# Performance work log

Hardware: AMD Instinct MI355X
Metric: run time of the kernel (lower is better)

## Reference

```python
import jax, jax.numpy as jnp
import numpy as np

N = 512  # DFT size, fixed by the module


def _dft_weights():
    # W[h, j] = exp(-2i*pi*j*h/N), same as the torch init loop
    h = np.arange(N).reshape(N, 1).astype(np.float64)
    j = np.arange(N).reshape(1, N).astype(np.float64)
    ang = -2.0 * np.pi * (h * j) / N
    return np.cos(ang).astype(np.float32), np.sin(ang).astype(np.float32)


def setup_inputs() -> dict:
    key = jax.random.key(0)
    k1, k2 = jax.random.split(key)
    shape = (8, 16, 256, N)  # (batch, channels, doppler, range_samples)
    x_re = jax.random.normal(k1, shape, dtype=jnp.float32)
    x_im = jax.random.normal(k2, shape, dtype=jnp.float32)
    w_re, w_im = _dft_weights()
    return {
        "x_re": x_re,
        "x_im": x_im,
        "w_re": jnp.asarray(w_re),
        "w_im": jnp.asarray(w_im),
    }


def reference(x_re, x_im, w_re, w_im):
    # CplxLinear without bias: y = x @ W^T, complex.
    # y_re = x_re @ Wr^T - x_im @ Wi^T ; y_im = x_re @ Wi^T + x_im @ Wr^T
    y_re = jnp.einsum('bcdj,hj->bcdh', x_re, w_re) - jnp.einsum('bcdj,hj->bcdh', x_im, w_im)
    y_im = jnp.einsum('bcdj,hj->bcdh', x_re, w_im) + jnp.einsum('bcdj,hj->bcdh', x_im, w_re)
    # stack real/imag on trailing axis (equivalent to torch.view_as_real layout)
    return jnp.stack([y_re, y_im], axis=-1)
```

## Files before the change

kernel.cpp:

```cpp
#include <hip/hip_runtime.h>

typedef __bf16 bf16_t;
typedef __bf16 bf16x8 __attribute__((ext_vector_type(8)));
typedef float f32x4 __attribute__((ext_vector_type(4)));
typedef unsigned int u32x4 __attribute__((ext_vector_type(4)));

#define KDIM 512
#define NDIM 512
#define BM 128
#define BN 128
#define BK 32

__device__ __forceinline__ void gld_lds16(const float* g, float* lds_uniform) {
  __builtin_amdgcn_global_load_lds(
      (const __attribute__((address_space(1))) void*)g,
      (__attribute__((address_space(3))) void*)lds_uniform, 16, 0, 0);
}

__device__ __forceinline__ bf16x8 neg8(bf16x8 v) {
  union { bf16x8 b; u32x4 u; } x;
  x.b = v;
  x.u = x.u ^ 0x80008000u;
  return x.b;
}

__device__ __forceinline__ bf16x8 afrag(const float* ldsx, int r, int h4) {
  const int base = r * 8;
  const int sw = r & 7;
  const float4 a = *(const float4*)(ldsx + 4 * (base + ((2 * h4) ^ sw)));
  const float4 b = *(const float4*)(ldsx + 4 * (base + ((2 * h4 + 1) ^ sw)));
  bf16x8 f;
  f[0] = (__bf16)a.x; f[1] = (__bf16)a.y; f[2] = (__bf16)a.z; f[3] = (__bf16)a.w;
  f[4] = (__bf16)b.x; f[5] = (__bf16)b.y; f[6] = (__bf16)b.z; f[7] = (__bf16)b.w;
  return f;
}

__device__ __forceinline__ bf16x8 pack8(float4 a, float4 b) {
  bf16x8 f;
  f[0] = (__bf16)a.x; f[1] = (__bf16)a.y; f[2] = (__bf16)a.z; f[3] = (__bf16)a.w;
  f[4] = (__bf16)b.x; f[5] = (__bf16)b.y; f[6] = (__bf16)b.z; f[7] = (__bf16)b.w;
  return f;
}

__global__ __launch_bounds__(256, 2) void dft_cgemm_kernel(
    const float* __restrict__ xr, const float* __restrict__ xi,
    const float* __restrict__ wre, const float* __restrict__ wim,
    float* __restrict__ out) {
  __shared__ __align__(16) float lds_xr[BM * BK];
  __shared__ __align__(16) float lds_xi[BM * BK];
  __shared__ __align__(16) bf16_t lds_wr[BN * BK];
  __shared__ __align__(16) bf16_t lds_wi[BN * BK];

  const int t = threadIdx.x;
  const int lane = t & 63;
  const int wv = t >> 6;

  const int b = blockIdx.x;
  const int xcd = b & 7;
  const int sidx = b >> 3;
  const int m0 = (xcd * 32 + (sidx >> 2)) * BM;
  const int n0 = (sidx & 3) * BN;

  const int wm = (wv >> 1) * 64;
  const int wn = (wv & 1) * 64;
  const int l16 = lane & 15;
  const int h4 = lane >> 4;

  const int wt15 = t & 15;
  const int wg = (t >> 4) & 3;

  f32x4 acc_re[4][4], acc_im[4][4];
#pragma unroll
  for (int i = 0; i < 4; ++i)
#pragma unroll
    for (int j = 0; j < 4; ++j) {
      acc_re[i][j] = (f32x4){0.f, 0.f, 0.f, 0.f};
      acc_im[i][j] = (f32x4){0.f, 0.f, 0.f, 0.f};
    }

  for (int k0 = 0; k0 < KDIM; k0 += BK) {
#pragma unroll
    for (int it = 0; it < 4; ++it) {
      const int S = it * 256 + t;
      const int row = S >> 3;
      const int g = (S & 7) ^ (row & 7);
      const size_t goff = (size_t)(m0 + row) * KDIM + k0 + g * 4;
      float* dst_r = lds_xr + 4 * (it * 256 + wv * 64);
      float* dst_i = lds_xi + 4 * (it * 256 + wv * 64);
      gld_lds16(xr + goff, dst_r);
      gld_lds16(xi + goff, dst_i);
    }
#pragma unroll
    for (int c = 0; c < 2; ++c) {
      const int row = (c * 4 + wv) * 16 + wt15;
      const float* gr = wre + (size_t)(n0 + row) * KDIM + k0 + wg * 8;
      const float* gi = wim + (size_t)(n0 + row) * KDIM + k0 + wg * 8;
      const float4 r0 = ((const float4*)gr)[0];
      const float4 r1 = ((const float4*)gr)[1];
      const float4 i0 = ((const float4*)gi)[0];
      const float4 i1 = ((const float4*)gi)[1];
      const int slot = c * 256 + t;
      *(bf16x8*)(lds_wr + slot * 8) = pack8(r0, r1);
      *(bf16x8*)(lds_wi + slot * 8) = pack8(i0, i1);
    }
    __syncthreads();

    bf16x8 ar[4], ai[4], br[4], bi[4], nbi[4];
#pragma unroll
    for (int mi = 0; mi < 4; ++mi) {
      const int r = wm + mi * 16 + l16;
      ar[mi] = afrag(lds_xr, r, h4);
      ai[mi] = afrag(lds_xi, r, h4);
    }
#pragma unroll
    for (int ni = 0; ni < 4; ++ni) {
      const int slot = ((wn >> 4) + ni) * 64 + h4 * 16 + l16;
      br[ni] = *(const bf16x8*)(lds_wr + slot * 8);
      bi[ni] = *(const bf16x8*)(lds_wi + slot * 8);
      nbi[ni] = neg8(bi[ni]);
    }
#pragma unroll
    for (int mi = 0; mi < 4; ++mi) {
#pragma unroll
      for (int ni = 0; ni < 4; ++ni) {
        acc_re[mi][ni] = __builtin_amdgcn_mfma_f32_16x16x32_bf16(ar[mi], br[ni], acc_re[mi][ni], 0, 0, 0);
        acc_im[mi][ni] = __builtin_amdgcn_mfma_f32_16x16x32_bf16(ar[mi], bi[ni], acc_im[mi][ni], 0, 0, 0);
        acc_re[mi][ni] = __builtin_amdgcn_mfma_f32_16x16x32_bf16(ai[mi], nbi[ni], acc_re[mi][ni], 0, 0, 0);
        acc_im[mi][ni] = __builtin_amdgcn_mfma_f32_16x16x32_bf16(ai[mi], br[ni], acc_im[mi][ni], 0, 0, 0);
      }
    }
    __syncthreads();
  }

#pragma unroll
  for (int mi = 0; mi < 4; ++mi) {
#pragma unroll
    for (int r = 0; r < 4; ++r) {
      const int m = m0 + wm + mi * 16 + h4 * 4 + r;
#pragma unroll
      for (int ni = 0; ni < 4; ++ni) {
        const int h = n0 + wn + ni * 16 + l16;
        float2 v;
        v.x = acc_re[mi][ni][r];
        v.y = acc_im[mi][ni][r];
        *(float2*)(out + ((size_t)m * NDIM + h) * 2) = v;
      }
    }
  }
}

extern "C" void kernel_launch(void* const* d_in, const int* in_sizes, int n_in,
                              void* d_out, int out_size, void* d_ws, size_t ws_size,
                              hipStream_t stream) {
  const float* xr  = (const float*)d_in[0];
  const float* xi  = (const float*)d_in[1];
  const float* wre = (const float*)d_in[2];
  const float* wim = (const float*)d_in[3];
  float* out = (float*)d_out;

  dim3 grid(1024);
  dim3 block(256);
  dft_cgemm_kernel<<<grid, block, 0, stream>>>(xr, xi, wre, wim, out);
}
```

Measured before the change: 293.8 us.

## Double-buffer X tiles in LDS and prefetch W into registers a step ahead

New measurement: 454.5 us. +54.7%, slower.

```diff
diff --git a/kernel.cpp b/kernel.cpp
--- a/kernel.cpp
+++ b/kernel.cpp
@@ -10,6 +10,7 @@
 #define BM 128
 #define BN 128
 #define BK 32
+#define NSTEP (KDIM / BK)
 
 __device__ __forceinline__ void gld_lds16(const float* g, float* lds_uniform) {
   __builtin_amdgcn_global_load_lds(
@@ -42,14 +43,14 @@
   return f;
 }
 
+struct Wregs { float4 r0, r1, i0, i1, r2, r3, i2, i3; };
+
 __global__ __launch_bounds__(256, 2) void dft_cgemm_kernel(
     const float* __restrict__ xr, const float* __restrict__ xi,
     const float* __restrict__ wre, const float* __restrict__ wim,
     float* __restrict__ out) {
-  __shared__ __align__(16) float lds_xr[BM * BK];
-  __shared__ __align__(16) float lds_xi[BM * BK];
-  __shared__ __align__(16) bf16_t lds_wr[BN * BK];
-  __shared__ __align__(16) bf16_t lds_wi[BN * BK];
+  __shared__ __align__(16) float  lds_x[2][2][BM * BK];
+  __shared__ __align__(16) bf16_t lds_w[2][BN * BK];
 
   const int t = threadIdx.x;
   const int lane = t & 63;
@@ -65,7 +66,6 @@
   const int wn = (wv & 1) * 64;
   const int l16 = lane & 15;
   const int h4 = lane >> 4;
-
   const int wt15 = t & 15;
   const int wg = (t >> 4) & 3;
 
@@ -78,45 +78,59 @@
       acc_im[i][j] = (f32x4){0.f, 0.f, 0.f, 0.f};
     }
 
-  for (int k0 = 0; k0 < KDIM; k0 += BK) {
+  auto stage_x = [&](int buf, int step) {
+    const int k0 = step * BK;
 #pragma unroll
     for (int it = 0; it < 4; ++it) {
       const int S = it * 256 + t;
       const int row = S >> 3;
       const int g = (S & 7) ^ (row & 7);
       const size_t goff = (size_t)(m0 + row) * KDIM + k0 + g * 4;
-      float* dst_r = lds_xr + 4 * (it * 256 + wv * 64);
-      float* dst_i = lds_xi + 4 * (it * 256 + wv * 64);
-      gld_lds16(xr + goff, dst_r);
-      gld_lds16(xi + goff, dst_i);
-    }
-#pragma unroll
-    for (int c = 0; c < 2; ++c) {
-      const int row = (c * 4 + wv) * 16 + wt15;
-      const float* gr = wre + (size_t)(n0 + row) * KDIM + k0 + wg * 8;
-      const float* gi = wim + (size_t)(n0 + row) * KDIM + k0 + wg * 8;
-      const float4 r0 = ((const float4*)gr)[0];
-      const float4 r1 = ((const float4*)gr)[1];
-      const float4 i0 = ((const float4*)gi)[0];
-      const float4 i1 = ((const float4*)gi)[1];
-      const int slot = c * 256 + t;
-      *(bf16x8*)(lds_wr + slot * 8) = pack8(r0, r1);
-      *(bf16x8*)(lds_wi + slot * 8) = pack8(i0, i1);
-    }
-    __syncthreads();
-
+      float* dr = &lds_x[buf][0][0] + 4 * (it * 256 + wv * 64);
+      float* di = &lds_x[buf][1][0] + 4 * (it * 256 + wv * 64);
+      gld_lds16(xr + goff, dr);
+      gld_lds16(xi + goff, di);
+    }
+  };
+
+  auto load_w = [&](int step) {
+    Wregs W;
+    const int k0 = step * BK;
+    const int row0 = wv * 16 + wt15;
+    const float* gr0 = wre + (size_t)(n0 + row0) * KDIM + k0 + wg * 8;
+    const float* gi0 = wim + (size_t)(n0 + row0) * KDIM + k0 + wg * 8;
+    W.r0 = ((const float4*)gr0)[0]; W.r1 = ((const float4*)gr0)[1];
+    W.i0 = ((const float4*)gi0)[0]; W.i1 = ((const float4*)gi0)[1];
+    const int row1 = 64 + wv * 16 + wt15;
+    const float* gr1 = wre + (size_t)(n0 + row1) * KDIM + k0 + wg * 8;
+    const float* gi1 = wim + (size_t)(n0 + row1) * KDIM + k0 + wg * 8;
+    W.r2 = ((const float4*)gr1)[0]; W.r3 = ((const float4*)gr1)[1];
+    W.i2 = ((const float4*)gi1)[0]; W.i3 = ((const float4*)gi1)[1];
+    return W;
+  };
+
+  auto write_w = [&](const Wregs& W) {
+    *(bf16x8*)(&lds_w[0][0] + (size_t)t * 8)         = pack8(W.r0, W.r1);
+    *(bf16x8*)(&lds_w[1][0] + (size_t)t * 8)         = pack8(W.i0, W.i1);
+    *(bf16x8*)(&lds_w[0][0] + (size_t)(256 + t) * 8) = pack8(W.r2, W.r3);
+    *(bf16x8*)(&lds_w[1][0] + (size_t)(256 + t) * 8) = pack8(W.i2, W.i3);
+  };
+
+  auto compute = [&](int buf) {
+    const float* ldsxr = &lds_x[buf][0][0];
+    const float* ldsxi = &lds_x[buf][1][0];
     bf16x8 ar[4], ai[4], br[4], bi[4], nbi[4];
 #pragma unroll
     for (int mi = 0; mi < 4; ++mi) {
       const int r = wm + mi * 16 + l16;
-      ar[mi] = afrag(lds_xr, r, h4);
-      ai[mi] = afrag(lds_xi, r, h4);
+      ar[mi] = afrag(ldsxr, r, h4);
+      ai[mi] = afrag(ldsxi, r, h4);
     }
 #pragma unroll
     for (int ni = 0; ni < 4; ++ni) {
       const int slot = ((wn >> 4) + ni) * 64 + h4 * 16 + l16;
-      br[ni] = *(const bf16x8*)(lds_wr + slot * 8);
-      bi[ni] = *(const bf16x8*)(lds_wi + slot * 8);
+      br[ni] = *(const bf16x8*)(&lds_w[0][0] + slot * 8);
+      bi[ni] = *(const bf16x8*)(&lds_w[1][0] + slot * 8);
       nbi[ni] = neg8(bi[ni]);
     }
 #pragma unroll
@@ -129,8 +143,52 @@
         acc_im[mi][ni] = __builtin_amdgcn_mfma_f32_16x16x32_bf16(ai[mi], br[ni], acc_im[mi][ni], 0, 0, 0);
       }
     }
-    __syncthreads();
+  };
+
+  Wregs Wp = load_w(0);
+  stage_x(0, 0);
+  write_w(Wp);
+  Wp = load_w(1);
+  stage_x(1, 1);
+  asm volatile("s_waitcnt vmcnt(16)" ::: "memory");
+  asm volatile("s_waitcnt lgkmcnt(0)" ::: "memory");
+  __builtin_amdgcn_s_barrier();
+  __builtin_amdgcn_sched_barrier(0);
+
+#pragma unroll 1
+  for (int tt = 0; tt < NSTEP - 2; tt += 2) {
+    compute(0);
+    __builtin_amdgcn_s_barrier();
+    __builtin_amdgcn_sched_barrier(0);
+    write_w(Wp);
+    Wp = load_w(tt + 2);
+    stage_x(0, tt + 2);
+    asm volatile("s_waitcnt vmcnt(16)" ::: "memory");
+    asm volatile("s_waitcnt lgkmcnt(0)" ::: "memory");
+    __builtin_amdgcn_s_barrier();
+    __builtin_amdgcn_sched_barrier(0);
+
+    compute(1);
+    __builtin_amdgcn_s_barrier();
+    __builtin_amdgcn_sched_barrier(0);
+    write_w(Wp);
+    Wp = load_w(tt + 3);
+    stage_x(1, tt + 3);
+    asm volatile("s_waitcnt vmcnt(16)" ::: "memory");
+    asm volatile("s_waitcnt lgkmcnt(0)" ::: "memory");
+    __builtin_amdgcn_s_barrier();
+    __builtin_amdgcn_sched_barrier(0);
   }
+
+  compute(0);
+  __builtin_amdgcn_s_barrier();
+  __builtin_amdgcn_sched_barrier(0);
+  write_w(Wp);
+  asm volatile("s_waitcnt vmcnt(0)" ::: "memory");
+  asm volatile("s_waitcnt lgkmcnt(0)" ::: "memory");
+  __builtin_amdgcn_s_barrier();
+  __builtin_amdgcn_sched_barrier(0);
+  compute(1);
 
 #pragma unroll
   for (int mi = 0; mi < 4; ++mi) {
```

## Load X fragments directly from global and stage W in larger K chunks

Applied to the files above, without the earlier changes.

After: 432.0 us. 47.1% more time.

```diff
diff --git a/kernel.cpp b/kernel.cpp
--- a/kernel.cpp
+++ b/kernel.cpp
@@ -10,29 +10,14 @@
 #define BM 128
 #define BN 128
 #define BK 32
-
-__device__ __forceinline__ void gld_lds16(const float* g, float* lds_uniform) {
-  __builtin_amdgcn_global_load_lds(
-      (const __attribute__((address_space(1))) void*)g,
-      (__attribute__((address_space(3))) void*)lds_uniform, 16, 0, 0);
-}
+#define KQ 128
+#define NQUART (KDIM / KQ)
 
 __device__ __forceinline__ bf16x8 neg8(bf16x8 v) {
   union { bf16x8 b; u32x4 u; } x;
   x.b = v;
   x.u = x.u ^ 0x80008000u;
   return x.b;
-}
-
-__device__ __forceinline__ bf16x8 afrag(const float* ldsx, int r, int h4) {
-  const int base = r * 8;
-  const int sw = r & 7;
-  const float4 a = *(const float4*)(ldsx + 4 * (base + ((2 * h4) ^ sw)));
-  const float4 b = *(const float4*)(ldsx + 4 * (base + ((2 * h4 + 1) ^ sw)));
-  bf16x8 f;
-  f[0] = (__bf16)a.x; f[1] = (__bf16)a.y; f[2] = (__bf16)a.z; f[3] = (__bf16)a.w;
-  f[4] = (__bf16)b.x; f[5] = (__bf16)b.y; f[6] = (__bf16)b.z; f[7] = (__bf16)b.w;
-  return f;
 }
 
 __device__ __forceinline__ bf16x8 pack8(float4 a, float4 b) {
@@ -46,10 +31,7 @@
     const float* __restrict__ xr, const float* __restrict__ xi,
     const float* __restrict__ wre, const float* __restrict__ wim,
     float* __restrict__ out) {
-  __shared__ __align__(16) float lds_xr[BM * BK];
-  __shared__ __align__(16) float lds_xi[BM * BK];
-  __shared__ __align__(16) bf16_t lds_wr[BN * BK];
-  __shared__ __align__(16) bf16_t lds_wi[BN * BK];
+  __shared__ __align__(16) bf16_t lds_w[2][BN * KQ];
 
   const int t = threadIdx.x;
   const int lane = t & 63;
@@ -65,9 +47,8 @@
   const int wn = (wv & 1) * 64;
   const int l16 = lane & 15;
   const int h4 = lane >> 4;
-
   const int wt15 = t & 15;
-  const int wg = (t >> 4) & 3;
+  const int wg16 = t >> 4;
 
   f32x4 acc_re[4][4], acc_im[4][4];
 #pragma unroll
@@ -78,58 +59,71 @@
       acc_im[i][j] = (f32x4){0.f, 0.f, 0.f, 0.f};
     }
 
-  for (int k0 = 0; k0 < KDIM; k0 += BK) {
+  auto stage_w = [&](int q) {
+    const int kq0 = q * KQ;
 #pragma unroll
-    for (int it = 0; it < 4; ++it) {
-      const int S = it * 256 + t;
-      const int row = S >> 3;
-      const int g = (S & 7) ^ (row & 7);
-      const size_t goff = (size_t)(m0 + row) * KDIM + k0 + g * 4;
-      float* dst_r = lds_xr + 4 * (it * 256 + wv * 64);
-      float* dst_i = lds_xi + 4 * (it * 256 + wv * 64);
-      gld_lds16(xr + goff, dst_r);
-      gld_lds16(xi + goff, dst_i);
-    }
-#pragma unroll
-    for (int c = 0; c < 2; ++c) {
-      const int row = (c * 4 + wv) * 16 + wt15;
-      const float* gr = wre + (size_t)(n0 + row) * KDIM + k0 + wg * 8;
-      const float* gi = wim + (size_t)(n0 + row) * KDIM + k0 + wg * 8;
+    for (int c = 0; c < 8; ++c) {
+      const int row = c * 16 + wt15;
+      const float* gr = wre + (size_t)(n0 + row) * KDIM + kq0 + wg16 * 8;
+      const float* gi = wim + (size_t)(n0 + row) * KDIM + kq0 + wg16 * 8;
       const float4 r0 = ((const float4*)gr)[0];
       const float4 r1 = ((const float4*)gr)[1];
       const float4 i0 = ((const float4*)gi)[0];
       const float4 i1 = ((const float4*)gi)[1];
       const int slot = c * 256 + t;
-      *(bf16x8*)(lds_wr + slot * 8) = pack8(r0, r1);
-      *(bf16x8*)(lds_wi + slot * 8) = pack8(i0, i1);
+      *(bf16x8*)(&lds_w[0][0] + (size_t)slot * 8) = pack8(r0, r1);
+      *(bf16x8*)(&lds_w[1][0] + (size_t)slot * 8) = pack8(i0, i1);
     }
-    __syncthreads();
+  };
 
-    bf16x8 ar[4], ai[4], br[4], bi[4], nbi[4];
+  stage_w(0);
+  __syncthreads();
+
+#pragma unroll 1
+  for (int q = 0; q < NQUART; ++q) {
 #pragma unroll
-    for (int mi = 0; mi < 4; ++mi) {
-      const int r = wm + mi * 16 + l16;
-      ar[mi] = afrag(lds_xr, r, h4);
-      ai[mi] = afrag(lds_xi, r, h4);
-    }
+    for (int ks = 0; ks < KQ / BK; ++ks) {
+      const int k0 = q * KQ + ks * BK;
+
+      bf16x8 ar[4], ai[4];
 #pragma unroll
-    for (int ni = 0; ni < 4; ++ni) {
-      const int slot = ((wn >> 4) + ni) * 64 + h4 * 16 + l16;
-      br[ni] = *(const bf16x8*)(lds_wr + slot * 8);
-      bi[ni] = *(const bf16x8*)(lds_wi + slot * 8);
-      nbi[ni] = neg8(bi[ni]);
-    }
-#pragma unroll
-    for (int mi = 0; mi < 4; ++mi) {
+      for (int mi = 0; mi < 4; ++mi) {
+        const size_t rbase =
+            (size_t)(m0 + wm + mi * 16 + l16) * KDIM + k0 + h4 * 8;
+        const float4 a0 = ((const float4*)(xr + rbase))[0];
+        const float4 a1 = ((const float4*)(xr + rbase))[1];
+        const float4 b0 = ((const float4*)(xi + rbase))[0];
+        const float4 b1 = ((const float4*)(xi + rbase))[1];
+        ar[mi] = pack8(a0, a1);
+        ai[mi] = pack8(b0, b1);
+      }
+
+      bf16x8 br[4], bi[4], nbi[4];
 #pragma unroll
       for (int ni = 0; ni < 4; ++ni) {
-        acc_re[mi][ni] = __builtin_amdgcn_mfma_f32_16x16x32_bf16(ar[mi], br[ni], acc_re[mi][ni], 0, 0, 0);
-        acc_im[mi][ni] = __builtin_amdgcn_mfma_f32_16x16x32_bf16(ar[mi], bi[ni], acc_im[mi][ni], 0, 0, 0);
-        acc_re[mi][ni] = __builtin_amdgcn_mfma_f32_16x16x32_bf16(ai[mi], nbi[ni], acc_re[mi][ni], 0, 0, 0);
-        acc_im[mi][ni] = __builtin_amdgcn_mfma_f32_16x16x32_bf16(ai[mi], br[ni], acc_im[mi][ni], 0, 0, 0);
+        const int slot = ((wn >> 4) + ni) * 256 + (ks * 4 + h4) * 16 + l16;
+        br[ni] = *(const bf16x8*)(&lds_w[0][0] + (size_t)slot * 8);
+        bi[ni] = *(const bf16x8*)(&lds_w[1][0] + (size_t)slot * 8);
+        nbi[ni] = neg8(bi[ni]);
+      }
+
+#pragma unroll
+      for (int mi = 0; mi < 4; ++mi) {
+#pragma unroll
+        for (int ni = 0; ni < 4; ++ni) {
+          acc_re[mi][ni] = __builtin_amdgcn_mfma_f32_16x16x32_bf16(ar[mi], br[ni], acc_re[mi][ni], 0, 0, 0);
+          acc_im[mi][ni] = __builtin_amdgcn_mfma_f32_16x16x32_bf16(ar[mi], bi[ni], acc_im[mi][ni], 0, 0, 0);
+          acc_re[mi][ni] = __builtin_amdgcn_mfma_f32_16x16x32_bf16(ai[mi], nbi[ni], acc_re[mi][ni], 0, 0, 0);
+          acc_im[mi][ni] = __builtin_amdgcn_mfma_f32_16x16x32_bf16(ai[mi], br[ni], acc_im[mi][ni], 0, 0, 0);
+        }
       }
     }
-    __syncthreads();
+
+    if (q + 1 < NQUART) {
+      __syncthreads();
+      stage_w(q + 1);
+      __syncthreads();
+    }
   }
 
 #pragma unroll
```

## Pre-pack DFT weights to bf16 and double-buffer LDS with async loads

Applied to the files above, without the earlier changes.

After: 317.8 us. +8.2%, slower.

```diff
diff --git a/kernel.cpp b/kernel.cpp
--- a/kernel.cpp
+++ b/kernel.cpp
@@ -10,6 +10,7 @@
 #define BM 128
 #define BN 128
 #define BK 32
+#define NSTEP (KDIM / BK)
 
 __device__ __forceinline__ void gld_lds16(const float* g, float* lds_uniform) {
   __builtin_amdgcn_global_load_lds(
@@ -24,25 +25,161 @@
   return x.b;
 }
 
+__device__ __forceinline__ bf16x8 pack8(float4 a, float4 b) {
+  bf16x8 f;
+  f[0] = (__bf16)a.x; f[1] = (__bf16)a.y; f[2] = (__bf16)a.z; f[3] = (__bf16)a.w;
+  f[4] = (__bf16)b.x; f[5] = (__bf16)b.y; f[6] = (__bf16)b.z; f[7] = (__bf16)b.w;
+  return f;
+}
+
 __device__ __forceinline__ bf16x8 afrag(const float* ldsx, int r, int h4) {
   const int base = r * 8;
   const int sw = r & 7;
   const float4 a = *(const float4*)(ldsx + 4 * (base + ((2 * h4) ^ sw)));
   const float4 b = *(const float4*)(ldsx + 4 * (base + ((2 * h4 + 1) ^ sw)));
-  bf16x8 f;
-  f[0] = (__bf16)a.x; f[1] = (__bf16)a.y; f[2] = (__bf16)a.z; f[3] = (__bf16)a.w;
-  f[4] = (__bf16)b.x; f[5] = (__bf16)b.y; f[6] = (__bf16)b.z; f[7] = (__bf16)b.w;
-  return f;
-}
-
-__device__ __forceinline__ bf16x8 pack8(float4 a, float4 b) {
-  bf16x8 f;
-  f[0] = (__bf16)a.x; f[1] = (__bf16)a.y; f[2] = (__bf16)a.z; f[3] = (__bf16)a.w;
-  f[4] = (__bf16)b.x; f[5] = (__bf16)b.y; f[6] = (__bf16)b.z; f[7] = (__bf16)b.w;
-  return f;
-}
-
-__global__ __launch_bounds__(256, 2) void dft_cgemm_kernel(
+  return pack8(a, b);
+}
+
+__global__ void dft_prep_w(const float* __restrict__ wre,
+                           const float* __restrict__ wim,
+                           bf16_t* __restrict__ wsw) {
+  const int gid = blockIdx.x * 256 + threadIdx.x;
+  const int comp = gid >> 15;
+  const int r15 = gid & 32767;
+  const int ntile = r15 >> 13;
+  const int r13 = r15 & 8191;
+  const int row = r13 >> 6;
+  const int sg = r13 & 63;
+  const int step = sg >> 2;
+  const int g = sg & 3;
+  const float* w = comp ? wim : wre;
+  const float* src = w + (size_t)(ntile * 128 + row) * KDIM + step * 32 + g * 8;
+  const float4 a = ((const float4*)src)[0];
+  const float4 b = ((const float4*)src)[1];
+  const int slot = (row >> 4) * 64 + g * 16 + (row & 15);
+  bf16_t* dst = wsw + ((((size_t)comp * 4 + ntile) * 16 + step) * 512 + slot) * 8;
+  *(bf16x8*)dst = pack8(a, b);
+}
+
+__global__ __launch_bounds__(512, 2) void dft_cgemm_kernel(
+    const float* __restrict__ xr, const float* __restrict__ xi,
+    const bf16_t* __restrict__ wsw, float* __restrict__ out) {
+  __shared__ __align__(16) float  lds_x[2][2][BM * BK];
+  __shared__ __align__(16) bf16_t lds_w[2][2][BN * BK];
+
+  const int t = threadIdx.x;
+  const int lane = t & 63;
+  const int wv = t >> 6;
+
+  const int b = blockIdx.x;
+  const int xcd = b & 7;
+  const int sidx = b >> 3;
+  const int nt = sidx & 3;
+  const int m0 = (xcd * 32 + (sidx >> 2)) * BM;
+  const int n0 = nt * BN;
+
+  const int wm = (wv >> 1) * 32;
+  const int wn = (wv & 1) * 64;
+  const int l16 = lane & 15;
+  const int h4 = lane >> 4;
+
+  f32x4 acc_re[2][4], acc_im[2][4];
+#pragma unroll
+  for (int i = 0; i < 2; ++i)
+#pragma unroll
+    for (int j = 0; j < 4; ++j) {
+      acc_re[i][j] = (f32x4){0.f, 0.f, 0.f, 0.f};
+      acc_im[i][j] = (f32x4){0.f, 0.f, 0.f, 0.f};
+    }
+
+  auto stage_x = [&](int buf, int step) {
+    const int k0 = step * BK;
+#pragma unroll
+    for (int comp = 0; comp < 2; ++comp) {
+      const float* src = comp ? xi : xr;
+#pragma unroll
+      for (int it = 0; it < 2; ++it) {
+        const int S = it * 512 + t;
+        const int row = S >> 3;
+        const int g = (S & 7) ^ (row & 7);
+        const size_t goff = (size_t)(m0 + row) * KDIM + k0 + g * 4;
+        float* dst = &lds_x[buf][comp][0] + 4 * (it * 512 + wv * 64);
+        gld_lds16(src + goff, dst);
+      }
+    }
+  };
+
+  auto stage_w = [&](int buf, int step) {
+#pragma unroll
+    for (int comp = 0; comp < 2; ++comp) {
+      const bf16_t* src =
+          wsw + ((((size_t)comp * 4 + nt) * 16 + step) * 512) * 8 + (size_t)t * 8;
+      float* dst = (float*)(&lds_w[buf][comp][0] + wv * 512);
+      gld_lds16((const float*)src, dst);
+    }
+  };
+
+  auto compute = [&](int buf) {
+    bf16x8 ar[2], ai[2];
+#pragma unroll
+    for (int mi = 0; mi < 2; ++mi) {
+      const int r = wm + mi * 16 + l16;
+      ar[mi] = afrag(&lds_x[buf][0][0], r, h4);
+      ai[mi] = afrag(&lds_x[buf][1][0], r, h4);
+    }
+    bf16x8 br[4], bi[4], nbi[4];
+#pragma unroll
+    for (int ni = 0; ni < 4; ++ni) {
+      const int slot = ((wn >> 4) + ni) * 64 + h4 * 16 + l16;
+      br[ni] = *(const bf16x8*)(&lds_w[buf][0][0] + slot * 8);
+      bi[ni] = *(const bf16x8*)(&lds_w[buf][1][0] + slot * 8);
+      nbi[ni] = neg8(bi[ni]);
+    }
+#pragma unroll
+    for (int mi = 0; mi < 2; ++mi) {
+#pragma unroll
+      for (int ni = 0; ni < 4; ++ni) {
+        acc_re[mi][ni] = __builtin_amdgcn_mfma_f32_16x16x32_bf16(ar[mi], br[ni], acc_re[mi][ni], 0, 0, 0);
+        acc_im[mi][ni] = __builtin_amdgcn_mfma_f32_16x16x32_bf16(ar[mi], bi[ni], acc_im[mi][ni], 0, 0, 0);
+        acc_re[mi][ni] = __builtin_amdgcn_mfma_f32_16x16x32_bf16(ai[mi], nbi[ni], acc_re[mi][ni], 0, 0, 0);
+        acc_im[mi][ni] = __builtin_amdgcn_mfma_f32_16x16x32_bf16(ai[mi], br[ni], acc_im[mi][ni], 0, 0, 0);
+      }
+    }
+  };
+
+  stage_x(0, 0);
+  stage_w(0, 0);
+  __syncthreads();
+
+#pragma unroll 1
+  for (int tt = 0; tt < NSTEP; ++tt) {
+    const int cur = tt & 1;
+    if (tt + 1 < NSTEP) {
+      stage_x(cur ^ 1, tt + 1);
+      stage_w(cur ^ 1, tt + 1);
+    }
+    compute(cur);
+    __syncthreads();
+  }
+
+#pragma unroll
+  for (int mi = 0; mi < 2; ++mi) {
+#pragma unroll
+    for (int r = 0; r < 4; ++r) {
+      const int m = m0 + wm + mi * 16 + h4 * 4 + r;
+#pragma unroll
+      for (int ni = 0; ni < 4; ++ni) {
+        const int h = n0 + wn + ni * 16 + l16;
+        float2 v;
+        v.x = acc_re[mi][ni][r];
+        v.y = acc_im[mi][ni][r];
+        *(float2*)(out + ((size_t)m * NDIM + h) * 2) = v;
+      }
+    }
+  }
+}
+
+__global__ __launch_bounds__(256, 2) void dft_cgemm_fallback(
     const float* __restrict__ xr, const float* __restrict__ xi,
     const float* __restrict__ wre, const float* __restrict__ wim,
     float* __restrict__ out) {
@@ -54,18 +191,15 @@
   const int t = threadIdx.x;
   const int lane = t & 63;
   const int wv = t >> 6;
-
   const int b = blockIdx.x;
   const int xcd = b & 7;
   const int sidx = b >> 3;
   const int m0 = (xcd * 32 + (sidx >> 2)) * BM;
   const int n0 = (sidx & 3) * BN;
-
   const int wm = (wv >> 1) * 64;
   const int wn = (wv & 1) * 64;
   const int l16 = lane & 15;
   const int h4 = lane >> 4;
-
   const int wt15 = t & 15;
   const int wg = (t >> 4) & 3;
 
@@ -158,7 +292,12 @@
   const float* wim = (const float*)d_in[3];
   float* out = (float*)d_out;
 
-  dim3 grid(1024);
-  dim3 block(256);
-  dft_cgemm_kernel<<<grid, block, 0, stream>>>(xr, xi, wre, wim, out);
-}
+  const size_t WS_NEED = (size_t)2 * 4 * 16 * 512 * 8 * sizeof(bf16_t);
+  if (d_ws != nullptr && ws_size >= WS_NEED) {
+    bf16_t* wsw = (bf16_t*)d_ws;
+    dft_prep_w<<<dim3(256), dim3(256), 0, stream>>>(wre, wim, wsw);
+    dft_cgemm_kernel<<<dim3(1024), dim3(512), 0, stream>>>(xr, xi, wsw, out);
+  } else {
+    dft_cgemm_fallback<<<dim3(1024), dim3(256), 0, stream>>>(xr, xi, wre, wim, out);
+  }
+}
```
